# Kernel tuning notes

Measured on AMD Instinct MI355X. Metric: run time of the kernel, lower is better.

Reference implementation:

```python
import jax, jax.numpy as jnp
import numpy as np

B, T, N, D, E = 16, 12, 512, 128, 32  # batch, time, nodes, model_dim, node_emb_dim


def setup_inputs() -> dict:
    key = jax.random.key(0)
    ks = jax.random.split(key, 7)
    return {
        "value": jax.random.normal(ks[0], (B, T, N, D), dtype=jnp.float32),
        "emb": jax.random.normal(ks[1], (T, N, E), dtype=jnp.float32),
        "attn_mask": jax.random.randint(ks[2], (B, N, N), 0, 2, dtype=jnp.int32),
        "W_qk": jax.random.normal(ks[3], (E, D), dtype=jnp.float32) * (1.0 / np.sqrt(E)),
        "b_qk": jax.random.normal(ks[4], (D,), dtype=jnp.float32) * 0.02,
        "W_v": jax.random.normal(ks[5], (D, D), dtype=jnp.float32) * (1.0 / np.sqrt(D)),
        "b_v": jax.random.normal(ks[6], (D,), dtype=jnp.float32) * 0.02,
    }


def reference(value, emb, attn_mask, W_qk, b_qk, W_v, b_v):
    # qk projection shared between query and key: [T, N, D]
    qk = emb @ W_qk + b_qk
    # query: softmax over feature dim D
    q = jax.nn.softmax(qk, axis=-1)                      # [T, N, D]
    # key: transpose then softmax over node dim N
    k = jax.nn.softmax(jnp.swapaxes(qk, -1, -2), axis=-1)  # [T, D, N]
    # value projection (note: out_proj in __init__ is unused in forward)
    v = value @ W_v + b_v                                # [B, T, N, D]
    # batch-independent base attention score, then broadcast over batch
    score = jnp.einsum('tnd,tdm->tnm', q, k)             # [T, N, N]
    score = jnp.broadcast_to(score[None], (value.shape[0],) + score.shape)  # [B, T, N, N]
    # masked fill: mask [B, N, N] -> [B, 1, N, N]
    score = jnp.where(attn_mask[:, None] == 0, jnp.float32(-1e9), score)
    out = jnp.einsum('btnm,btmd->btnd', score, v)         # [B, T, N, D]
    return out
```

## Files before the change

### kernel.cpp

```cpp
#include <hip/hip_runtime.h>

#define B_ 16
#define T_ 12
#define N_ 512
#define D_ 128
#define E_ 32

typedef __attribute__((ext_vector_type(8))) unsigned short u16x8;
typedef __attribute__((ext_vector_type(8))) __bf16 bf16x8;
typedef __attribute__((ext_vector_type(4))) float f32x4;

static __device__ __forceinline__ unsigned short f2bf(float f) {
    unsigned u = __float_as_uint(f);
    unsigned r = (u + 0x7fffu + ((u >> 16) & 1u)) >> 16;
    return (unsigned short)r;
}

__global__ __launch_bounds__(128) void kA1(const float* __restrict__ emb,
                                           const float* __restrict__ Wqk,
                                           const float* __restrict__ bqk,
                                           float* __restrict__ qk,
                                           unsigned short* __restrict__ qb) {
    int tn = blockIdx.x;
    int d  = threadIdx.x;
    __shared__ float es[E_];
    if (d < E_) es[d] = emb[tn * E_ + d];
    __syncthreads();
    float acc = bqk[d];
#pragma unroll
    for (int e = 0; e < E_; ++e) acc = fmaf(es[e], Wqk[e * D_ + d], acc);
    qk[(size_t)tn * D_ + d] = acc;

    __shared__ float red[D_];
    red[d] = acc;
    __syncthreads();
#pragma unroll
    for (int s = 64; s > 0; s >>= 1) {
        if (d < s) red[d] = fmaxf(red[d], red[d + s]);
        __syncthreads();
    }
    float mx = red[0];
    __syncthreads();
    float ex = __expf(acc - mx);
    red[d] = ex;
    __syncthreads();
#pragma unroll
    for (int s = 64; s > 0; s >>= 1) {
        if (d < s) red[d] += red[d + s];
        __syncthreads();
    }
    qb[(size_t)tn * D_ + d] = f2bf(ex / red[0]);
}

__global__ __launch_bounds__(256) void kA2n(const float* __restrict__ qk,
                                            unsigned short* __restrict__ kN) {
    int t = blockIdx.x >> 2;
    int d0 = (blockIdx.x & 3) * 32;
    int tid = threadIdx.x;
    int dc = tid & 31, ni = tid >> 5;
    const float* base = qk + (size_t)t * N_ * D_ + d0 + dc;
    float vals[64];
    float mx = -1e30f;
#pragma unroll
    for (int j = 0; j < 64; ++j) {
        vals[j] = base[(size_t)(ni + 8 * j) * D_];
        mx = fmaxf(mx, vals[j]);
    }
    __shared__ float red[8][33];
    red[ni][dc] = mx;
    __syncthreads();
    if (ni == 0) {
        float m = red[0][dc];
#pragma unroll
        for (int r = 1; r < 8; ++r) m = fmaxf(m, red[r][dc]);
        red[0][dc] = m;
    }
    __syncthreads();
    mx = red[0][dc];
    float sum = 0.f;
#pragma unroll
    for (int j = 0; j < 64; ++j) {
        vals[j] = __expf(vals[j] - mx);
        sum += vals[j];
    }
    __syncthreads();
    red[ni][dc] = sum;
    __syncthreads();
    if (ni == 0) {
        float s = red[0][dc];
#pragma unroll
        for (int r = 1; r < 8; ++r) s += red[r][dc];
        red[0][dc] = s;
    }
    __syncthreads();
    float inv = 1.f / red[0][dc];
    unsigned short* op = kN + (size_t)t * N_ * D_ + d0 + dc;
#pragma unroll
    for (int j = 0; j < 64; ++j)
        op[(size_t)(ni + 8 * j) * D_] = f2bf(vals[j] * inv);
}

__global__ __launch_bounds__(256) void kW(const float* __restrict__ Wv,
                                          unsigned short* __restrict__ WvT) {
    int i = blockIdx.x * 256 + threadIdx.x;
    int d = i >> 7, k = i & 127;
    WvT[d * 128 + k] = f2bf(Wv[k * 128 + d]);
}

__global__ __launch_bounds__(256) void kA3m(const unsigned short* __restrict__ qb,
                                            const unsigned short* __restrict__ kN,
                                            unsigned short* __restrict__ sc) {
    int mt = blockIdx.x, nt = blockIdx.y, t = blockIdx.z;
    int n0 = nt * 128, m0 = mt * 128;
    int tid = threadIdx.x;
    int wave = tid >> 6, lane = tid & 63;
    int q = lane >> 4, lr = lane & 15;
    int rbase = (wave & 1) * 64, cbase = (wave >> 1) * 64;

    __shared__ unsigned short Qs[128 * 72];
    __shared__ unsigned short Ks[128 * 72];

    const unsigned short* qp = qb + (size_t)t * N_ * D_ + (size_t)n0 * D_;
    const unsigned short* kp = kN + (size_t)t * N_ * D_ + (size_t)m0 * D_;

    f32x4 acc[4][4];
#pragma unroll
    for (int i = 0; i < 4; ++i)
#pragma unroll
        for (int j = 0; j < 4; ++j) acc[i][j] = (f32x4){0.f, 0.f, 0.f, 0.f};

    for (int c = 0; c < 2; ++c) {
        int k0 = c * 64;
        __syncthreads();
#pragma unroll
        for (int i = 0; i < 4; ++i) {
            int lin = tid + i * 256;
            int r = lin >> 3, seg = lin & 7;
            *(u16x8*)&Qs[r * 72 + seg * 8] =
                *(const u16x8*)&qp[(size_t)r * D_ + k0 + seg * 8];
            *(u16x8*)&Ks[r * 72 + seg * 8] =
                *(const u16x8*)&kp[(size_t)r * D_ + k0 + seg * 8];
        }
        __syncthreads();
#pragma unroll
        for (int kk = 0; kk < 2; ++kk) {
            bf16x8 a[4], b[4];
#pragma unroll
            for (int i = 0; i < 4; ++i)
                a[i] = *(const bf16x8*)&Qs[(rbase + 16 * i + lr) * 72 + kk * 32 + q * 8];
#pragma unroll
            for (int j = 0; j < 4; ++j)
                b[j] = *(const bf16x8*)&Ks[(cbase + 16 * j + lr) * 72 + kk * 32 + q * 8];
#pragma unroll
            for (int i = 0; i < 4; ++i)
#pragma unroll
                for (int j = 0; j < 4; ++j)
                    acc[i][j] = __builtin_amdgcn_mfma_f32_16x16x32_bf16(
                        a[i], b[j], acc[i][j], 0, 0, 0);
        }
    }
    unsigned short* sp = sc + (size_t)t * N_ * N_;
#pragma unroll
    for (int i = 0; i < 4; ++i)
#pragma unroll
        for (int j = 0; j < 4; ++j) {
            int row0 = n0 + rbase + 16 * i + q * 4;
            int col = m0 + cbase + 16 * j + lr;
#pragma unroll
            for (int e = 0; e < 4; ++e)
                sp[(size_t)(row0 + e) * N_ + col] = f2bf(acc[i][j][e]);
        }
}

__global__ __launch_bounds__(256) void kM(const int* __restrict__ mask,
                                          unsigned* __restrict__ mb) {
    int o = blockIdx.x * 256 + threadIdx.x;
    const int* mp = mask + (size_t)o * 32;
    unsigned bits = 0;
#pragma unroll
    for (int j = 0; j < 32; j += 4) {
        int4 m4 = *(const int4*)&mp[j];
        bits |= (m4.x ? 1u : 0u) << j;
        bits |= (m4.y ? 1u : 0u) << (j + 1);
        bits |= (m4.z ? 1u : 0u) << (j + 2);
        bits |= (m4.w ? 1u : 0u) << (j + 3);
    }
    mb[o] = bits;
}

__global__ __launch_bounds__(256) void kBm(const float* __restrict__ value,
                                           const unsigned short* __restrict__ WvT,
                                           const float* __restrict__ bv,
                                           unsigned short* __restrict__ vT) {
    int mt = blockIdx.x, bt = blockIdx.y;
    int m0 = mt * 128;
    int tid = threadIdx.x;
    int wave = tid >> 6, lane = tid & 63;
    int q = lane >> 4, lr = lane & 15;
    int rbase = (wave & 1) * 64, cbase = (wave >> 1) * 64;

    __shared__ unsigned short Ws[128 * 72];
    __shared__ unsigned short Vs[128 * 72];

    const float* vp = value + ((size_t)bt * N_ + m0) * D_;

    f32x4 acc[4][4];
#pragma unroll
    for (int i = 0; i < 4; ++i)
#pragma unroll
        for (int j = 0; j < 4; ++j) acc[i][j] = (f32x4){0.f, 0.f, 0.f, 0.f};

    for (int c = 0; c < 2; ++c) {
        int k0 = c * 64;
        __syncthreads();
#pragma unroll
        for (int i = 0; i < 4; ++i) {
            int lin = tid + i * 256;
            int r = lin >> 3, seg = lin & 7;
            *(u16x8*)&Ws[r * 72 + seg * 8] =
                *(const u16x8*)&WvT[r * 128 + k0 + seg * 8];
        }
#pragma unroll
        for (int i = 0; i < 8; ++i) {
            int lin = tid + i * 256;
            int r = lin >> 4, c4 = lin & 15;
            float4 f = *(const float4*)&vp[(size_t)r * D_ + k0 + c4 * 4];
            ushort4 o;
            o.x = f2bf(f.x); o.y = f2bf(f.y); o.z = f2bf(f.z); o.w = f2bf(f.w);
            *(ushort4*)&Vs[r * 72 + c4 * 4] = o;
        }
        __syncthreads();
#pragma unroll
        for (int kk = 0; kk < 2; ++kk) {
            bf16x8 a[4], b[4];
#pragma unroll
            for (int i = 0; i < 4; ++i)
                a[i] = *(const bf16x8*)&Ws[(rbase + 16 * i + lr) * 72 + kk * 32 + q * 8];
#pragma unroll
            for (int j = 0; j < 4; ++j)
                b[j] = *(const bf16x8*)&Vs[(cbase + 16 * j + lr) * 72 + kk * 32 + q * 8];
#pragma unroll
            for (int i = 0; i < 4; ++i)
#pragma unroll
                for (int j = 0; j < 4; ++j)
                    acc[i][j] = __builtin_amdgcn_mfma_f32_16x16x32_bf16(
                        a[i], b[j], acc[i][j], 0, 0, 0);
        }
    }
    unsigned short* op = vT + (size_t)bt * N_ * D_;
#pragma unroll
    for (int i = 0; i < 4; ++i) {
        int row0 = rbase + 16 * i + q * 4;
#pragma unroll
        for (int j = 0; j < 4; ++j) {
            int col = m0 + cbase + 16 * j + lr;
#pragma unroll
            for (int e = 0; e < 4; ++e)
                op[(size_t)(row0 + e) * N_ + col] = f2bf(acc[i][j][e] + bv[row0 + e]);
        }
    }
}

__global__ __launch_bounds__(256) void kC(const unsigned short* __restrict__ sc,
                                          const unsigned* __restrict__ mb,
                                          const unsigned short* __restrict__ vT,
                                          float* __restrict__ out) {
    int n0 = blockIdx.x * 128;
    int t = blockIdx.y, b = blockIdx.z;
    int tid = threadIdx.x;
    int wave = tid >> 6, lane = tid & 63;
    int q = lane >> 4, lr = lane & 15;
    int rbase = (wave & 1) * 64;
    int cbase = (wave >> 1) * 64;

    __shared__ unsigned short Ss[128 * 40];
    __shared__ unsigned short Vs[128 * 40];

    const unsigned short* scp = sc + (size_t)t * N_ * N_ + (size_t)n0 * N_;
    const unsigned short* vtp = vT + ((size_t)(b * T_ + t)) * N_ * D_;
    const unsigned* mbp = mb + ((size_t)b * N_ + n0) * 16;

    const unsigned short NEG = 0xCE6E;

    f32x4 acc[4][4];
#pragma unroll
    for (int i = 0; i < 4; ++i)
#pragma unroll
        for (int j = 0; j < 4; ++j) acc[i][j] = (f32x4){0.f, 0.f, 0.f, 0.f};

    int sr = tid >> 1, sh = tid & 1;

    for (int kc = 0; kc < 16; ++kc) {
        int m0 = kc * 32;
        const unsigned short* g = scp + (size_t)sr * N_ + m0 + sh * 16;
        u16x8 s0 = *(const u16x8*)g;
        u16x8 s1 = *(const u16x8*)(g + 8);
        unsigned bits = mbp[sr * 16 + kc] >> (sh * 16);
        u16x8 o0, o1;
#pragma unroll
        for (int j = 0; j < 8; ++j) {
            o0[j] = ((bits >> j) & 1u) ? s0[j] : NEG;
            o1[j] = ((bits >> (j + 8)) & 1u) ? s1[j] : NEG;
        }
        *(u16x8*)&Ss[sr * 40 + sh * 16]     = o0;
        *(u16x8*)&Ss[sr * 40 + sh * 16 + 8] = o1;
#pragma unroll
        for (int i = 0; i < 2; ++i) {
            int lin = tid + i * 256;
            int d = lin >> 2, qq = lin & 3;
            *(u16x8*)&Vs[d * 40 + qq * 8] =
                *(const u16x8*)&vtp[(size_t)d * N_ + m0 + qq * 8];
        }
        __syncthreads();
        bf16x8 a[4], bfr[4];
#pragma unroll
        for (int i = 0; i < 4; ++i)
            a[i] = *(const bf16x8*)&Ss[(rbase + 16 * i + lr) * 40 + q * 8];
#pragma unroll
        for (int j = 0; j < 4; ++j)
            bfr[j] = *(const bf16x8*)&Vs[(cbase + 16 * j + lr) * 40 + q * 8];
#pragma unroll
        for (int i = 0; i < 4; ++i)
#pragma unroll
            for (int j = 0; j < 4; ++j)
                acc[i][j] = __builtin_amdgcn_mfma_f32_16x16x32_bf16(
                    a[i], bfr[j], acc[i][j], 0, 0, 0);
        __syncthreads();
    }

    float* ob = out + ((size_t)(b * T_ + t)) * N_ * D_;
#pragma unroll
    for (int i = 0; i < 4; ++i) {
#pragma unroll
        for (int j = 0; j < 4; ++j) {
            int row0 = n0 + rbase + 16 * i + q * 4;
            int col = cbase + 16 * j + lr;
#pragma unroll
            for (int e = 0; e < 4; ++e)
                ob[(size_t)(row0 + e) * D_ + col] = acc[i][j][e];
        }
    }
}

extern "C" void kernel_launch(void* const* d_in, const int* in_sizes, int n_in,
                              void* d_out, int out_size, void* d_ws, size_t ws_size,
                              hipStream_t stream) {
    const float* value = (const float*)d_in[0];
    const float* emb   = (const float*)d_in[1];
    const int*   mask  = (const int*)d_in[2];
    const float* Wqk   = (const float*)d_in[3];
    const float* bqk   = (const float*)d_in[4];
    const float* Wv    = (const float*)d_in[5];
    const float* bvv   = (const float*)d_in[6];
    float* out = (float*)d_out;

    float* ws = (float*)d_ws;
    float*          qkf  = ws;
    unsigned short* qb   = (unsigned short*)(ws + 786432);
    unsigned short* kNb  = (unsigned short*)(ws + 1179648);
    unsigned short* scb  = (unsigned short*)(ws + 1572864);
    unsigned short* vtb  = (unsigned short*)(ws + 3145728);
    unsigned short* WvTb = (unsigned short*)(ws + 9437184);
    unsigned*       mbp  = (unsigned*)(ws + 9445376);

    kA1<<<T_ * N_, 128, 0, stream>>>(emb, Wqk, bqk, qkf, qb);
    kA2n<<<48, 256, 0, stream>>>(qkf, kNb);
    kW<<<64, 256, 0, stream>>>(Wv, WvTb);
    kA3m<<<dim3(4, 4, T_), 256, 0, stream>>>(qb, kNb, scb);
    kM<<<512, 256, 0, stream>>>(mask, mbp);
    kBm<<<dim3(4, B_ * T_), 256, 0, stream>>>(value, WvTb, bvv, vtb);
    kC<<<dim3(4, T_, B_), 256, 0, stream>>>(scb, mbp, vtb, out);
}
```

Measured before the change: 178.1 us.

## Merge small prep kernels, widen key-softmax grid, and prefetch register tiles in kC

Folds the Wv transpose into the qk projection kernel and merges the score GEMM, value projection and mask bit-packing into one heterogeneous launch. This cuts the launch count from seven to four. The key-softmax kernel now runs on 192 blocks of 8 columns instead of 48 blocks of 32, for more parallelism. The final score×V kernel now uses 64-wide K chunks, preloads the next chunk into registers while the MFMAs run, and syncs once per iteration. The cost is higher register and LDS use per block, plus branch divergence in the merged kernel.

```diff
diff --git a/kernel.cpp b/kernel.cpp
--- a/kernel.cpp
+++ b/kernel.cpp
@@ -16,11 +16,19 @@
     return (unsigned short)r;
 }
 
-__global__ __launch_bounds__(128) void kA1(const float* __restrict__ emb,
-                                           const float* __restrict__ Wqk,
-                                           const float* __restrict__ bqk,
-                                           float* __restrict__ qk,
-                                           unsigned short* __restrict__ qb) {
+__global__ __launch_bounds__(128) void kA1W(const float* __restrict__ emb,
+                                            const float* __restrict__ Wqk,
+                                            const float* __restrict__ bqk,
+                                            float* __restrict__ qk,
+                                            unsigned short* __restrict__ qb,
+                                            const float* __restrict__ Wv,
+                                            unsigned short* __restrict__ WvT) {
+    if (blockIdx.x >= 6144) {
+        int i = (blockIdx.x - 6144) * 128 + threadIdx.x;
+        int d = i >> 7, k = i & 127;
+        WvT[d * 128 + k] = f2bf(Wv[k * 128 + d]);
+        return;
+    }
     int tn = blockIdx.x;
     int d  = threadIdx.x;
     __shared__ float es[E_];
@@ -54,209 +62,199 @@
 
 __global__ __launch_bounds__(256) void kA2n(const float* __restrict__ qk,
                                             unsigned short* __restrict__ kN) {
-    int t = blockIdx.x >> 2;
-    int d0 = (blockIdx.x & 3) * 32;
+    int t = blockIdx.x >> 4;
+    int d0 = (blockIdx.x & 15) * 8;
     int tid = threadIdx.x;
-    int dc = tid & 31, ni = tid >> 5;
+    int dc = tid & 7, ni = tid >> 3;
     const float* base = qk + (size_t)t * N_ * D_ + d0 + dc;
-    float vals[64];
+    float vals[16];
     float mx = -1e30f;
 #pragma unroll
-    for (int j = 0; j < 64; ++j) {
-        vals[j] = base[(size_t)(ni + 8 * j) * D_];
+    for (int j = 0; j < 16; ++j) {
+        vals[j] = base[(size_t)(ni + 32 * j) * D_];
         mx = fmaxf(mx, vals[j]);
     }
-    __shared__ float red[8][33];
+    __shared__ float red[32][9];
     red[ni][dc] = mx;
     __syncthreads();
-    if (ni == 0) {
-        float m = red[0][dc];
-#pragma unroll
-        for (int r = 1; r < 8; ++r) m = fmaxf(m, red[r][dc]);
-        red[0][dc] = m;
+    if (tid < 8) {
+        float m = red[0][tid];
+#pragma unroll
+        for (int r = 1; r < 32; ++r) m = fmaxf(m, red[r][tid]);
+        red[0][tid] = m;
     }
     __syncthreads();
     mx = red[0][dc];
     float sum = 0.f;
 #pragma unroll
-    for (int j = 0; j < 64; ++j) {
+    for (int j = 0; j < 16; ++j) {
         vals[j] = __expf(vals[j] - mx);
         sum += vals[j];
     }
     __syncthreads();
     red[ni][dc] = sum;
     __syncthreads();
-    if (ni == 0) {
-        float s = red[0][dc];
-#pragma unroll
-        for (int r = 1; r < 8; ++r) s += red[r][dc];
-        red[0][dc] = s;
+    if (tid < 8) {
+        float s = red[0][tid];
+#pragma unroll
+        for (int r = 1; r < 32; ++r) s += red[r][tid];
+        red[0][tid] = s;
     }
     __syncthreads();
     float inv = 1.f / red[0][dc];
     unsigned short* op = kN + (size_t)t * N_ * D_ + d0 + dc;
 #pragma unroll
-    for (int j = 0; j < 64; ++j)
-        op[(size_t)(ni + 8 * j) * D_] = f2bf(vals[j] * inv);
-}
-
-__global__ __launch_bounds__(256) void kW(const float* __restrict__ Wv,
-                                          unsigned short* __restrict__ WvT) {
-    int i = blockIdx.x * 256 + threadIdx.x;
-    int d = i >> 7, k = i & 127;
-    WvT[d * 128 + k] = f2bf(Wv[k * 128 + d]);
-}
-
-__global__ __launch_bounds__(256) void kA3m(const unsigned short* __restrict__ qb,
-                                            const unsigned short* __restrict__ kN,
-                                            unsigned short* __restrict__ sc) {
-    int mt = blockIdx.x, nt = blockIdx.y, t = blockIdx.z;
-    int n0 = nt * 128, m0 = mt * 128;
+    for (int j = 0; j < 16; ++j)
+        op[(size_t)(ni + 32 * j) * D_] = f2bf(vals[j] * inv);
+}
+
+__global__ __launch_bounds__(256) void kF(const unsigned short* __restrict__ qb,
+                                          const unsigned short* __restrict__ kN,
+                                          unsigned short* __restrict__ sc,
+                                          const float* __restrict__ value,
+                                          const unsigned short* __restrict__ WvT,
+                                          const float* __restrict__ bv,
+                                          unsigned short* __restrict__ vT,
+                                          const int* __restrict__ mask,
+                                          unsigned* __restrict__ mb) {
+    __shared__ unsigned short shl[2][128 * 72];
+    int bid = blockIdx.x;
     int tid = threadIdx.x;
+
+    if (bid >= 960) {
+        int o = (bid - 960) * 256 + tid;
+        const int* mp = mask + (size_t)o * 32;
+        unsigned bits = 0;
+#pragma unroll
+        for (int j = 0; j < 32; j += 4) {
+            int4 m4 = *(const int4*)&mp[j];
+            bits |= (m4.x ? 1u : 0u) << j;
+            bits |= (m4.y ? 1u : 0u) << (j + 1);
+            bits |= (m4.z ? 1u : 0u) << (j + 2);
+            bits |= (m4.w ? 1u : 0u) << (j + 3);
+        }
+        mb[o] = bits;
+        return;
+    }
+
     int wave = tid >> 6, lane = tid & 63;
     int q = lane >> 4, lr = lane & 15;
     int rbase = (wave & 1) * 64, cbase = (wave >> 1) * 64;
 
-    __shared__ unsigned short Qs[128 * 72];
-    __shared__ unsigned short Ks[128 * 72];
-
-    const unsigned short* qp = qb + (size_t)t * N_ * D_ + (size_t)n0 * D_;
-    const unsigned short* kp = kN + (size_t)t * N_ * D_ + (size_t)m0 * D_;
-
     f32x4 acc[4][4];
 #pragma unroll
     for (int i = 0; i < 4; ++i)
 #pragma unroll
         for (int j = 0; j < 4; ++j) acc[i][j] = (f32x4){0.f, 0.f, 0.f, 0.f};
 
-    for (int c = 0; c < 2; ++c) {
-        int k0 = c * 64;
-        __syncthreads();
+    if (bid < 192) {
+        int mt = bid & 3, nt = (bid >> 2) & 3, t = bid >> 4;
+        int n0 = nt * 128, m0 = mt * 128;
+        unsigned short* Qs = shl[0];
+        unsigned short* Ks = shl[1];
+        const unsigned short* qp = qb + (size_t)t * N_ * D_ + (size_t)n0 * D_;
+        const unsigned short* kp = kN + (size_t)t * N_ * D_ + (size_t)m0 * D_;
+
+        for (int c = 0; c < 2; ++c) {
+            int k0 = c * 64;
+            __syncthreads();
+#pragma unroll
+            for (int i = 0; i < 4; ++i) {
+                int lin = tid + i * 256;
+                int r = lin >> 3, seg = lin & 7;
+                *(u16x8*)&Qs[r * 72 + seg * 8] =
+                    *(const u16x8*)&qp[(size_t)r * D_ + k0 + seg * 8];
+                *(u16x8*)&Ks[r * 72 + seg * 8] =
+                    *(const u16x8*)&kp[(size_t)r * D_ + k0 + seg * 8];
+            }
+            __syncthreads();
+#pragma unroll
+            for (int kk = 0; kk < 2; ++kk) {
+                bf16x8 a[4], b[4];
+#pragma unroll
+                for (int i = 0; i < 4; ++i)
+                    a[i] = *(const bf16x8*)&Qs[(rbase + 16 * i + lr) * 72 + kk * 32 + q * 8];
+#pragma unroll
+                for (int j = 0; j < 4; ++j)
+                    b[j] = *(const bf16x8*)&Ks[(cbase + 16 * j + lr) * 72 + kk * 32 + q * 8];
+#pragma unroll
+                for (int i = 0; i < 4; ++i)
+#pragma unroll
+                    for (int j = 0; j < 4; ++j)
+                        acc[i][j] = __builtin_amdgcn_mfma_f32_16x16x32_bf16(
+                            a[i], b[j], acc[i][j], 0, 0, 0);
+            }
+        }
+        unsigned short* sp = sc + (size_t)t * N_ * N_;
+#pragma unroll
+        for (int i = 0; i < 4; ++i)
+#pragma unroll
+            for (int j = 0; j < 4; ++j) {
+                int row0 = n0 + rbase + 16 * i + q * 4;
+                int col = m0 + cbase + 16 * j + lr;
+#pragma unroll
+                for (int e = 0; e < 4; ++e)
+                    sp[(size_t)(row0 + e) * N_ + col] = f2bf(acc[i][j][e]);
+            }
+        return;
+    }
+
+    {
+        int idx = bid - 192;
+        int mt = idx & 3, bt = idx >> 2;
+        int m0 = mt * 128;
+        unsigned short* Ws = shl[0];
+        unsigned short* Vs = shl[1];
+        const float* vp = value + ((size_t)bt * N_ + m0) * D_;
+
+        for (int c = 0; c < 2; ++c) {
+            int k0 = c * 64;
+            __syncthreads();
+#pragma unroll
+            for (int i = 0; i < 4; ++i) {
+                int lin = tid + i * 256;
+                int r = lin >> 3, seg = lin & 7;
+                *(u16x8*)&Ws[r * 72 + seg * 8] =
+                    *(const u16x8*)&WvT[r * 128 + k0 + seg * 8];
+            }
+#pragma unroll
+            for (int i = 0; i < 8; ++i) {
+                int lin = tid + i * 256;
+                int r = lin >> 4, c4 = lin & 15;
+                float4 f = *(const float4*)&vp[(size_t)r * D_ + k0 + c4 * 4];
+                ushort4 o;
+                o.x = f2bf(f.x); o.y = f2bf(f.y); o.z = f2bf(f.z); o.w = f2bf(f.w);
+                *(ushort4*)&Vs[r * 72 + c4 * 4] = o;
+            }
+            __syncthreads();
+#pragma unroll
+            for (int kk = 0; kk < 2; ++kk) {
+                bf16x8 a[4], b[4];
+#pragma unroll
+                for (int i = 0; i < 4; ++i)
+                    a[i] = *(const bf16x8*)&Ws[(rbase + 16 * i + lr) * 72 + kk * 32 + q * 8];
+#pragma unroll
+                for (int j = 0; j < 4; ++j)
+                    b[j] = *(const bf16x8*)&Vs[(cbase + 16 * j + lr) * 72 + kk * 32 + q * 8];
+#pragma unroll
+                for (int i = 0; i < 4; ++i)
+#pragma unroll
+                    for (int j = 0; j < 4; ++j)
+                        acc[i][j] = __builtin_amdgcn_mfma_f32_16x16x32_bf16(
+                            a[i], b[j], acc[i][j], 0, 0, 0);
+            }
+        }
+        unsigned short* op = vT + (size_t)bt * N_ * D_;
 #pragma unroll
         for (int i = 0; i < 4; ++i) {
-            int lin = tid + i * 256;
-            int r = lin >> 3, seg = lin & 7;
-            *(u16x8*)&Qs[r * 72 + seg * 8] =
-                *(const u16x8*)&qp[(size_t)r * D_ + k0 + seg * 8];
-            *(u16x8*)&Ks[r * 72 + seg * 8] =
-                *(const u16x8*)&kp[(size_t)r * D_ + k0 + seg * 8];
-        }
-        __syncthreads();
-#pragma unroll
-        for (int kk = 0; kk < 2; ++kk) {
-            bf16x8 a[4], b[4];
-#pragma unroll
-            for (int i = 0; i < 4; ++i)
-                a[i] = *(const bf16x8*)&Qs[(rbase + 16 * i + lr) * 72 + kk * 32 + q * 8];
-#pragma unroll
-            for (int j = 0; j < 4; ++j)
-                b[j] = *(const bf16x8*)&Ks[(cbase + 16 * j + lr) * 72 + kk * 32 + q * 8];
-#pragma unroll
-            for (int i = 0; i < 4; ++i)
-#pragma unroll
-                for (int j = 0; j < 4; ++j)
-                    acc[i][j] = __builtin_amdgcn_mfma_f32_16x16x32_bf16(
-                        a[i], b[j], acc[i][j], 0, 0, 0);
-        }
-    }
-    unsigned short* sp = sc + (size_t)t * N_ * N_;
-#pragma unroll
-    for (int i = 0; i < 4; ++i)
-#pragma unroll
-        for (int j = 0; j < 4; ++j) {
-            int row0 = n0 + rbase + 16 * i + q * 4;
-            int col = m0 + cbase + 16 * j + lr;
-#pragma unroll
-            for (int e = 0; e < 4; ++e)
-                sp[(size_t)(row0 + e) * N_ + col] = f2bf(acc[i][j][e]);
-        }
-}
-
-__global__ __launch_bounds__(256) void kM(const int* __restrict__ mask,
-                                          unsigned* __restrict__ mb) {
-    int o = blockIdx.x * 256 + threadIdx.x;
-    const int* mp = mask + (size_t)o * 32;
-    unsigned bits = 0;
-#pragma unroll
-    for (int j = 0; j < 32; j += 4) {
-        int4 m4 = *(const int4*)&mp[j];
-        bits |= (m4.x ? 1u : 0u) << j;
-        bits |= (m4.y ? 1u : 0u) << (j + 1);
-        bits |= (m4.z ? 1u : 0u) << (j + 2);
-        bits |= (m4.w ? 1u : 0u) << (j + 3);
-    }
-    mb[o] = bits;
-}
-
-__global__ __launch_bounds__(256) void kBm(const float* __restrict__ value,
-                                           const unsigned short* __restrict__ WvT,
-                                           const float* __restrict__ bv,
-                                           unsigned short* __restrict__ vT) {
-    int mt = blockIdx.x, bt = blockIdx.y;
-    int m0 = mt * 128;
-    int tid = threadIdx.x;
-    int wave = tid >> 6, lane = tid & 63;
-    int q = lane >> 4, lr = lane & 15;
-    int rbase = (wave & 1) * 64, cbase = (wave >> 1) * 64;
-
-    __shared__ unsigned short Ws[128 * 72];
-    __shared__ unsigned short Vs[128 * 72];
-
-    const float* vp = value + ((size_t)bt * N_ + m0) * D_;
-
-    f32x4 acc[4][4];
-#pragma unroll
-    for (int i = 0; i < 4; ++i)
-#pragma unroll
-        for (int j = 0; j < 4; ++j) acc[i][j] = (f32x4){0.f, 0.f, 0.f, 0.f};
-
-    for (int c = 0; c < 2; ++c) {
-        int k0 = c * 64;
-        __syncthreads();
-#pragma unroll
-        for (int i = 0; i < 4; ++i) {
-            int lin = tid + i * 256;
-            int r = lin >> 3, seg = lin & 7;
-            *(u16x8*)&Ws[r * 72 + seg * 8] =
-                *(const u16x8*)&WvT[r * 128 + k0 + seg * 8];
-        }
-#pragma unroll
-        for (int i = 0; i < 8; ++i) {
-            int lin = tid + i * 256;
-            int r = lin >> 4, c4 = lin & 15;
-            float4 f = *(const float4*)&vp[(size_t)r * D_ + k0 + c4 * 4];
-            ushort4 o;
-            o.x = f2bf(f.x); o.y = f2bf(f.y); o.z = f2bf(f.z); o.w = f2bf(f.w);
-            *(ushort4*)&Vs[r * 72 + c4 * 4] = o;
-        }
-        __syncthreads();
-#pragma unroll
-        for (int kk = 0; kk < 2; ++kk) {
-            bf16x8 a[4], b[4];
-#pragma unroll
-            for (int i = 0; i < 4; ++i)
-                a[i] = *(const bf16x8*)&Ws[(rbase + 16 * i + lr) * 72 + kk * 32 + q * 8];
-#pragma unroll
-            for (int j = 0; j < 4; ++j)
-                b[j] = *(const bf16x8*)&Vs[(cbase + 16 * j + lr) * 72 + kk * 32 + q * 8];
-#pragma unroll
-            for (int i = 0; i < 4; ++i)
-#pragma unroll
-                for (int j = 0; j < 4; ++j)
-                    acc[i][j] = __builtin_amdgcn_mfma_f32_16x16x32_bf16(
-                        a[i], b[j], acc[i][j], 0, 0, 0);
-        }
-    }
-    unsigned short* op = vT + (size_t)bt * N_ * D_;
-#pragma unroll
-    for (int i = 0; i < 4; ++i) {
-        int row0 = rbase + 16 * i + q * 4;
-#pragma unroll
-        for (int j = 0; j < 4; ++j) {
-            int col = m0 + cbase + 16 * j + lr;
-#pragma unroll
-            for (int e = 0; e < 4; ++e)
-                op[(size_t)(row0 + e) * N_ + col] = f2bf(acc[i][j][e] + bv[row0 + e]);
+            int row0 = rbase + 16 * i + q * 4;
+#pragma unroll
+            for (int j = 0; j < 4; ++j) {
+                int col = m0 + cbase + 16 * j + lr;
+#pragma unroll
+                for (int e = 0; e < 4; ++e)
+                    op[(size_t)(row0 + e) * N_ + col] = f2bf(acc[i][j][e] + bv[row0 + e]);
+            }
         }
     }
 }
@@ -270,11 +268,10 @@
     int tid = threadIdx.x;
     int wave = tid >> 6, lane = tid & 63;
     int q = lane >> 4, lr = lane & 15;
-    int rbase = (wave & 1) * 64;
-    int cbase = (wave >> 1) * 64;
-
-    __shared__ unsigned short Ss[128 * 40];
-    __shared__ unsigned short Vs[128 * 40];
+    int rbase = (wave & 1) * 64, cbase = (wave >> 1) * 64;
+
+    __shared__ unsigned short Ss[128 * 72];
+    __shared__ unsigned short Vs[128 * 72];
 
     const unsigned short* scp = sc + (size_t)t * N_ * N_ + (size_t)n0 * N_;
     const unsigned short* vtp = vT + ((size_t)(b * T_ + t)) * N_ * D_;
@@ -288,44 +285,60 @@
 #pragma unroll
         for (int j = 0; j < 4; ++j) acc[i][j] = (f32x4){0.f, 0.f, 0.f, 0.f};
 
-    int sr = tid >> 1, sh = tid & 1;
-
-    for (int kc = 0; kc < 16; ++kc) {
-        int m0 = kc * 32;
-        const unsigned short* g = scp + (size_t)sr * N_ + m0 + sh * 16;
-        u16x8 s0 = *(const u16x8*)g;
-        u16x8 s1 = *(const u16x8*)(g + 8);
-        unsigned bits = mbp[sr * 16 + kc] >> (sh * 16);
-        u16x8 o0, o1;
-#pragma unroll
-        for (int j = 0; j < 8; ++j) {
-            o0[j] = ((bits >> j) & 1u) ? s0[j] : NEG;
-            o1[j] = ((bits >> (j + 8)) & 1u) ? s1[j] : NEG;
-        }
-        *(u16x8*)&Ss[sr * 40 + sh * 16]     = o0;
-        *(u16x8*)&Ss[sr * 40 + sh * 16 + 8] = o1;
-#pragma unroll
-        for (int i = 0; i < 2; ++i) {
-            int lin = tid + i * 256;
-            int d = lin >> 2, qq = lin & 3;
-            *(u16x8*)&Vs[d * 40 + qq * 8] =
-                *(const u16x8*)&vtp[(size_t)d * N_ + m0 + qq * 8];
+    int sr = tid >> 1, sh2 = tid & 1;
+    const unsigned short* sg = scp + (size_t)sr * N_ + sh2 * 32;
+    const unsigned short* vg = vtp + (size_t)sr * N_ + sh2 * 32;
+    const unsigned* mwp = mbp + sr * 16 + sh2;
+
+    u16x8 sreg[4], vreg[4];
+    unsigned mw;
+#pragma unroll
+    for (int p = 0; p < 4; ++p) {
+        sreg[p] = *(const u16x8*)(sg + p * 8);
+        vreg[p] = *(const u16x8*)(vg + p * 8);
+    }
+    mw = mwp[0];
+
+    for (int kc = 0; kc < 8; ++kc) {
+        if (kc) __syncthreads();
+        unsigned short* Sd = &Ss[sr * 72 + sh2 * 32];
+        unsigned short* Vd = &Vs[sr * 72 + sh2 * 32];
+#pragma unroll
+        for (int p = 0; p < 4; ++p) {
+            unsigned bits = mw >> (p * 8);
+            u16x8 o;
+#pragma unroll
+            for (int j = 0; j < 8; ++j)
+                o[j] = ((bits >> j) & 1u) ? sreg[p][j] : NEG;
+            *(u16x8*)(Sd + p * 8) = o;
+            *(u16x8*)(Vd + p * 8) = vreg[p];
         }
         __syncthreads();
-        bf16x8 a[4], bfr[4];
-#pragma unroll
-        for (int i = 0; i < 4; ++i)
-            a[i] = *(const bf16x8*)&Ss[(rbase + 16 * i + lr) * 40 + q * 8];
-#pragma unroll
-        for (int j = 0; j < 4; ++j)
-            bfr[j] = *(const bf16x8*)&Vs[(cbase + 16 * j + lr) * 40 + q * 8];
-#pragma unroll
-        for (int i = 0; i < 4; ++i)
+        if (kc < 7) {
+            int off = (kc + 1) * 64;
+#pragma unroll
+            for (int p = 0; p < 4; ++p) {
+                sreg[p] = *(const u16x8*)(sg + off + p * 8);
+                vreg[p] = *(const u16x8*)(vg + off + p * 8);
+            }
+            mw = mwp[(kc + 1) * 2];
+        }
+#pragma unroll
+        for (int ks = 0; ks < 2; ++ks) {
+            bf16x8 a[4], bfr[4];
+#pragma unroll
+            for (int i = 0; i < 4; ++i)
+                a[i] = *(const bf16x8*)&Ss[(rbase + 16 * i + lr) * 72 + ks * 32 + q * 8];
 #pragma unroll
             for (int j = 0; j < 4; ++j)
-                acc[i][j] = __builtin_amdgcn_mfma_f32_16x16x32_bf16(
-                    a[i], bfr[j], acc[i][j], 0, 0, 0);
-        __syncthreads();
+                bfr[j] = *(const bf16x8*)&Vs[(cbase + 16 * j + lr) * 72 + ks * 32 + q * 8];
+#pragma unroll
+            for (int i = 0; i < 4; ++i)
+#pragma unroll
+                for (int j = 0; j < 4; ++j)
+                    acc[i][j] = __builtin_amdgcn_mfma_f32_16x16x32_bf16(
+                        a[i], bfr[j], acc[i][j], 0, 0, 0);
+        }
     }
 
     float* ob = out + ((size_t)(b * T_ + t)) * N_ * D_;
@@ -363,11 +376,8 @@
     unsigned short* WvTb = (unsigned short*)(ws + 9437184);
     unsigned*       mbp  = (unsigned*)(ws + 9445376);
 
-    kA1<<<T_ * N_, 128, 0, stream>>>(emb, Wqk, bqk, qkf, qb);
-    kA2n<<<48, 256, 0, stream>>>(qkf, kNb);
-    kW<<<64, 256, 0, stream>>>(Wv, WvTb);
-    kA3m<<<dim3(4, 4, T_), 256, 0, stream>>>(qb, kNb, scb);
-    kM<<<512, 256, 0, stream>>>(mask, mbp);
-    kBm<<<dim3(4, B_ * T_), 256, 0, stream>>>(value, WvTb, bvv, vtb);
+    kA1W<<<6272, 128, 0, stream>>>(emb, Wqk, bqk, qkf, qb, Wv, WvTb);
+    kA2n<<<192, 256, 0, stream>>>(qkf, kNb);
+    kF<<<1472, 256, 0, stream>>>(qb, kNb, scb, value, WvTb, bvv, vtb, mask, mbp);
     kC<<<dim3(4, T_, B_), 256, 0, stream>>>(scb, mbp, vtb, out);
 }
```

Result: faster. 167.1 us (-6.2%).
